# Optimization experiments

Hardware: AMD Instinct MI355X
Metric: run time of the kernel (lower is better)

## Reference

```python
import jax, jax.numpy as jnp
import numpy as np

HNUM = 64; WNUM = 64; TNUM = 2048; BIN_LEN = 0.01
B = 64; P = 512; VD = 128
VAP = 2.0; MINZ = 0.0; MAXZ = 2.0
LASER_ORIGIN = jnp.array([0.0, 0.0, -1.0], dtype=jnp.float32)
CAMERA_ORIGIN = jnp.array([0.05, 0.0, -1.0], dtype=jnp.float32)


def _wall_grid():
    ys = jnp.linspace(-1.0, 1.0, HNUM, dtype=jnp.float32)
    xs = jnp.linspace(-1.0, 1.0, WNUM, dtype=jnp.float32)
    gx, gy = jnp.meshgrid(xs, ys)  # [H, W]
    return jnp.stack([gx, gy, jnp.zeros_like(gx)], axis=-1)  # [H, W, 3] on wall z=0


def _normalize(v):
    n = jnp.linalg.norm(v, axis=-1, keepdims=True)
    return v / jnp.maximum(n, 1e-12)


def grid_sample_3d(vol, grid):
    # vol [D,H,W]; grid [N,3] (x,y,z) in [-1,1]; trilinear, zeros padding, align_corners=True
    D, H, W = vol.shape
    fx = (grid[:, 0] + 1.0) * 0.5 * (W - 1)
    fy = (grid[:, 1] + 1.0) * 0.5 * (H - 1)
    fz = (grid[:, 2] + 1.0) * 0.5 * (D - 1)
    x0 = jnp.floor(fx); y0 = jnp.floor(fy); z0 = jnp.floor(fz)
    wx = fx - x0; wy = fy - y0; wz = fz - z0
    x0 = x0.astype(jnp.int32); y0 = y0.astype(jnp.int32); z0 = z0.astype(jnp.int32)
    out = jnp.zeros(grid.shape[0], dtype=vol.dtype)
    for dz in (0, 1):
        for dy in (0, 1):
            for dx in (0, 1):
                ix = x0 + dx; iy = y0 + dy; iz = z0 + dz
                valid = (ix >= 0) & (ix < W) & (iy >= 0) & (iy < H) & (iz >= 0) & (iz < D)
                v = vol[jnp.clip(iz, 0, D - 1), jnp.clip(iy, 0, H - 1), jnp.clip(ix, 0, W - 1)]
                w = (wx if dx else 1.0 - wx) * (wy if dy else 1.0 - wy) * (wz if dz else 1.0 - wz)
                out = out + jnp.where(valid, v, 0.0) * w
    return out


def _forward(surf_pos, surf_normals, xys, phasor_volume, params_albedo,
             param_scale, param_sigma, param_lamda, param_dc):
    y_idx = xys[:, 0, 0]
    x_idx = xys[:, 0, 1]
    wall = _wall_grid()
    laser_pos = wall; camera_pos = wall
    d1 = jnp.linalg.norm(laser_pos - LASER_ORIGIN, axis=-1)  # [H,W]
    d4 = jnp.linalg.norm(camera_pos - CAMERA_ORIGIN, axis=-1)

    # --- albedo volume -> trilinear gather at surface points ---
    mask = (jax.lax.stop_gradient(phasor_volume) > 0.0).astype(jnp.float32)
    albedo_vol = jnp.clip(params_albedo * mask + phasor_volume * mask, 0.0, 1.0)
    z_scale = 2.0 / (MAXZ - MINZ)
    z_off = z_scale * (-MINZ) - 1.0
    g = jnp.stack([surf_pos[..., 0] * (2.0 / VAP),
                   -surf_pos[..., 1] * (2.0 / VAP),
                   surf_pos[..., 2] * z_scale + z_off], axis=-1).reshape(-1, 3)
    albedo_interp = grid_sample_3d(jnp.transpose(albedo_vol, (2, 0, 1)), g)
    albedo_interp = albedo_interp.reshape(surf_pos.shape[0], surf_pos.shape[1])  # [B,P]

    # --- per-point radiometry ---
    lp = laser_pos[y_idx, x_idx][:, None, :]   # [B,1,3]
    cp = camera_pos[y_idx, x_idx][:, None, :]
    lv = lp - surf_pos
    ld = jnp.linalg.norm(lv, axis=-1)          # [B,P]
    lvn = _normalize(lv)
    sv = cp - surf_pos
    sd = jnp.linalg.norm(sv, axis=-1)
    svn = _normalize(sv)
    # wall_normal = [0,0,1] => dot(v, n) = v_z
    value = (param_scale * albedo_interp / (ld ** 2 * sd ** 2)
             * (-lvn[..., 2]) * (-svn[..., 2])
             * jnp.sum(lvn * surf_normals, axis=-1)
             * jnp.sum(svn * surf_normals, axis=-1))  # [B,P]

    dist = d1[y_idx, x_idx][:, None] + ld + sd + d4[y_idx, x_idx][:, None]  # [B,P]
    axis_t = jnp.arange(TNUM, dtype=jnp.float32) * BIN_LEN
    sig2 = BIN_LEN ** 2 / (8.0 * np.log(2.0))
    # Gaussian splat of each point's time-of-flight into the transient histogram
    tdata = jnp.sum(value[..., None]
                    * jnp.exp(-(axis_t - dist[..., None]) ** 2 / (2.0 * sig2)), axis=1)  # [B,T]

    # --- impulse response: gaussian jitter (x) exponential SPAD response ---
    knum = TNUM // 4
    at = jnp.arange(knum, dtype=jnp.float32) - knum // 2
    sinv = 1.0 / param_sigma
    gauss = (sinv * (1.0 / jnp.sqrt(2.0 * jnp.pi))
             * jnp.exp(-at ** 2 * sinv ** 2 / 2.0))
    atc = jnp.maximum(at, 0.0)
    resp = param_lamda * jnp.exp(-param_lamda * atc)
    resp = jnp.where(jnp.arange(knum) < knum // 2, 0.0, resp)
    ir = jnp.convolve(gauss, resp, mode='same')
    tdata_out = jax.vmap(lambda r: jnp.convolve(r, ir, mode='same'))(tdata) + param_dc
    return tdata_out, tdata


def setup_inputs() -> dict:
    key = jax.random.key(0)
    k1, k2, k3, k4, k5 = jax.random.split(key, 5)
    sp = jax.random.uniform(k1, (B, P, 3), dtype=jnp.float32)
    surf_pos = sp * jnp.array([2.0, 2.0, 1.6]) + jnp.array([-1.0, -1.0, 0.2])
    surf_normals = jax.random.normal(k2, (B, P, 3), dtype=jnp.float32)
    surf_normals = surf_normals / jnp.maximum(
        jnp.linalg.norm(surf_normals, axis=-1, keepdims=True), 1e-12)
    xys = jax.random.randint(k3, (B, 1, 2), 0, HNUM).astype(jnp.int64)
    phasor_volume = jax.random.uniform(k4, (HNUM, WNUM, VD), dtype=jnp.float32)
    params_albedo = 0.1 * jax.random.uniform(k5, (HNUM, WNUM, VD), dtype=jnp.float32)
    return {
        'surf_pos': surf_pos,
        'surf_normals': surf_normals,
        'xys': xys,
        'phasor_volume': phasor_volume,
        'params_albedo': params_albedo,
        'param_scale': jnp.ones((1,), jnp.float32),
        'param_sigma': 0.8917 * jnp.ones((1,), jnp.float32),
        'param_lamda': 0.5 * jnp.ones((1,), jnp.float32),
        'param_dc': 1e-4 * jnp.ones((1,), jnp.float32),
    }


def reference(surf_pos, surf_normals, xys, phasor_volume, params_albedo,
              param_scale, param_sigma, param_lamda, param_dc):
    return _forward(surf_pos, surf_normals, xys, phasor_volume, params_albedo,
                    param_scale, param_sigma, param_lamda, param_dc)
```

## Files before the change

kernel.cpp:

```cpp
#include <hip/hip_runtime.h>
#include <math.h>

#define HNUM 64
#define WNUM 64
#define TNUM 2048
#define B_   64
#define P_   512
#define VD_  128
#define NSPLIT 4
#define NTAP 128
#define KOFF 240

#define LOG2E 1.44269504088896340736f

__global__ __launch_bounds__(128) void ptr_scatter_kernel(
    const float* __restrict__ surf_pos,
    const float* __restrict__ surf_norm,
    const int*   __restrict__ xys,
    const float* __restrict__ phasor,
    const float* __restrict__ albedo_p,
    const float* __restrict__ scale_p,
    const float* __restrict__ sigma_p,
    const float* __restrict__ lamda_p,
    float* __restrict__ ws)
{
    __shared__ float s_h[2048];
    const int tid = threadIdx.x;
    const int blk = blockIdx.x;

    if (blk == B_ * NSPLIT) {
        float* sA = s_h;
        float* sB = s_h + 128;
        const float sinv = 1.0f / sigma_p[0];
        const float lam  = lamda_p[0];
        const float eneg = __builtin_amdgcn_exp2f(-lam * LOG2E);
        const float at = (float)(tid - 17);
        const float g  = sinv * 0.3989422804014327f *
                         __builtin_amdgcn_exp2f(-0.5f * LOG2E * at * at * sinv * sinv);
        sA[tid] = (tid == 0) ? 0.0f : eneg;
        sB[tid] = lam * g;
        __syncthreads();
        #pragma unroll
        for (int d = 1; d < NTAP; d <<= 1) {
            float a = sA[tid], b = sB[tid], al = 1.0f, bl = 0.0f;
            if (tid >= d) { al = sA[tid - d]; bl = sB[tid - d]; }
            __syncthreads();
            if (tid >= d) { sA[tid] = a * al; sB[tid] = fmaf(a, bl, b); }
            __syncthreads();
        }
        ws[tid] = sB[tid];
        return;
    }

    const int b = blk >> 2, q = blk & 3;
    #pragma unroll
    for (int s = 0; s < 4; ++s)
        *reinterpret_cast<float4*>(&s_h[(tid + s * 128) * 4]) =
            make_float4(0.0f, 0.0f, 0.0f, 0.0f);
    __syncthreads();

    {
        const int p = q * 128 + tid;
        const int base = (b * P_ + p) * 3;
        const float px = surf_pos[base + 0];
        const float py = surf_pos[base + 1];
        const float pz = surf_pos[base + 2];
        const float nx = surf_norm[base + 0];
        const float ny = surf_norm[base + 1];
        const float nz = surf_norm[base + 2];

        const int y = xys[b * 2 + 0];
        const int x = xys[b * 2 + 1];
        const float wxp = -1.0f + 2.0f * (float)x / 63.0f;
        const float wyp = -1.0f + 2.0f * (float)y / 63.0f;
        const float d1  = sqrtf(wxp * wxp + wyp * wyp + 1.0f);
        const float dxc = wxp - 0.05f;
        const float d4  = sqrtf(dxc * dxc + wyp * wyp + 1.0f);
        const float scale = scale_p[0];

        const float fx = (px + 1.0f) * 31.5f;
        const float fy = (1.0f - py) * 31.5f;
        const float fz = pz * 63.5f;
        const float x0f = floorf(fx), y0f = floorf(fy), z0f = floorf(fz);
        const float wwx = fx - x0f, wwy = fy - y0f, wwz = fz - z0f;
        const int ix0 = (int)x0f, iy0 = (int)y0f, iz0 = (int)z0f;
        const int ix1 = min(ix0 + 1, WNUM - 1);
        const int iy1 = min(iy0 + 1, HNUM - 1);
        const int iz1 = iz0 + 1;

        float interp = 0.0f;
        #pragma unroll
        for (int c = 0; c < 8; ++c) {
            const int dx = c & 1, dy = (c >> 1) & 1, dz = c >> 2;
            const int ix = dx ? ix1 : ix0;
            const int iy = dy ? iy1 : iy0;
            const int iz = dz ? iz1 : iz0;
            const int idx = (iy * WNUM + ix) * VD_ + iz;
            const float ph = phasor[idx];
            const float al = albedo_p[idx];
            const float v  = (ph > 0.0f) ? fminf(fmaxf(al + ph, 0.0f), 1.0f) : 0.0f;
            const float w3 = (dx ? wwx : 1.0f - wwx) *
                             (dy ? wwy : 1.0f - wwy) *
                             (dz ? wwz : 1.0f - wwz);
            interp = fmaf(v, w3, interp);
        }

        const float lvx = wxp - px, lvy = wyp - py, lvz = -pz;
        const float ld2 = lvx * lvx + lvy * lvy + lvz * lvz;
        const float ld  = sqrtf(ld2);
        const float ild = 1.0f / fmaxf(ld, 1e-12f);
        const float lnz = lvz * ild;
        const float dotn = (lvx * nx + lvy * ny + lvz * nz) * ild;
        const float value = scale * interp / (ld2 * ld2) * (lnz * lnz) * (dotn * dotn);
        const float dist  = d1 + 2.0f * ld + d4;

        const float tc = dist * 100.0f;
        const int it0 = (int)floorf(tc) - 3;
        #pragma unroll
        for (int k = 0; k < 8; ++k) {
            const int t = it0 + k;
            if (t >= 0 && t < TNUM) {
                const float db = (float)t - tc;
                const float w = __builtin_amdgcn_exp2f(-4.0f * db * db);
                atomicAdd(&s_h[t], value * w);
            }
        }
    }
    __syncthreads();

    float* dst = ws + NTAP + blk * 2048;
    #pragma unroll
    for (int s = 0; s < 4; ++s) {
        const int i4 = (tid + s * 128) * 4;
        *reinterpret_cast<float4*>(&dst[i4]) =
            *reinterpret_cast<const float4*>(&s_h[i4]);
    }
}

__global__ __launch_bounds__(128) void ptr_conv_kernel(
    const float* __restrict__ ws,
    const float* __restrict__ dc_p,
    float* __restrict__ out,
    float* __restrict__ tdata)
{
    __shared__ float s_w[640];
    const int tid = threadIdx.x;
    const int b  = blockIdx.x >> 2;
    const int T0 = (blockIdx.x & 3) << 9;

    const float* part = ws + NTAP + (b * NSPLIT) * 2048;
    for (int idx = tid; idx < 160; idx += 128) {
        const int i = idx * 4;
        const int g = T0 - 112 + i;
        float4 v = make_float4(0.0f, 0.0f, 0.0f, 0.0f);
        if (g >= 0 && g < TNUM) {
            const float4 v0 = *reinterpret_cast<const float4*>(&part[g]);
            const float4 v1 = *reinterpret_cast<const float4*>(&part[2048 + g]);
            const float4 v2 = *reinterpret_cast<const float4*>(&part[4096 + g]);
            const float4 v3 = *reinterpret_cast<const float4*>(&part[6144 + g]);
            v.x = (v0.x + v1.x) + (v2.x + v3.x);
            v.y = (v0.y + v1.y) + (v2.y + v3.y);
            v.z = (v0.z + v1.z) + (v2.z + v3.z);
            v.w = (v0.w + v1.w) + (v2.w + v3.w);
        }
        *reinterpret_cast<float4*>(&s_w[i]) = v;
    }
    __syncthreads();

    const int l0 = tid * 4;
    *reinterpret_cast<float4*>(&tdata[b * TNUM + T0 + l0]) =
        *reinterpret_cast<const float4*>(&s_w[112 + l0]);

    const float4* irt4 = reinterpret_cast<const float4*>(ws);
    float acc0 = 0.0f, acc1 = 0.0f, acc2 = 0.0f, acc3 = 0.0f;
    float4 hi = *reinterpret_cast<const float4*>(&s_w[l0 + 128]);
    #pragma unroll
    for (int c = 0; c < 32; ++c) {
        const float4 lo  = *reinterpret_cast<const float4*>(&s_w[l0 + 124 - 4 * c]);
        const float4 irv = irt4[c];
        acc0 = fmaf(irv.x, lo.w, acc0); acc1 = fmaf(irv.x, hi.x, acc1);
        acc2 = fmaf(irv.x, hi.y, acc2); acc3 = fmaf(irv.x, hi.z, acc3);
        acc0 = fmaf(irv.y, lo.z, acc0); acc1 = fmaf(irv.y, lo.w, acc1);
        acc2 = fmaf(irv.y, hi.x, acc2); acc3 = fmaf(irv.y, hi.y, acc3);
        acc0 = fmaf(irv.z, lo.y, acc0); acc1 = fmaf(irv.z, lo.z, acc1);
        acc2 = fmaf(irv.z, lo.w, acc2); acc3 = fmaf(irv.z, hi.x, acc3);
        acc0 = fmaf(irv.w, lo.x, acc0); acc1 = fmaf(irv.w, lo.y, acc1);
        acc2 = fmaf(irv.w, lo.z, acc2); acc3 = fmaf(irv.w, lo.w, acc3);
        hi = lo;
    }

    const float dc = dc_p[0];
    float4 o;
    o.x = acc0 + dc; o.y = acc1 + dc; o.z = acc2 + dc; o.w = acc3 + dc;
    *reinterpret_cast<float4*>(&out[b * TNUM + T0 + l0]) = o;
}

extern "C" void kernel_launch(void* const* d_in, const int* in_sizes, int n_in,
                              void* d_out, int out_size, void* d_ws, size_t ws_size,
                              hipStream_t stream) {
    const float* surf_pos  = (const float*)d_in[0];
    const float* surf_norm = (const float*)d_in[1];
    const int*   xys       = (const int*)  d_in[2];
    const float* phasor    = (const float*)d_in[3];
    const float* albedo    = (const float*)d_in[4];
    const float* scale_p   = (const float*)d_in[5];
    const float* sigma_p   = (const float*)d_in[6];
    const float* lamda_p   = (const float*)d_in[7];
    const float* dc_p      = (const float*)d_in[8];

    float* out   = (float*)d_out;
    float* tdata = out + B_ * TNUM;
    float* ws    = (float*)d_ws;

    ptr_scatter_kernel<<<B_ * NSPLIT + 1, 128, 0, stream>>>(
        surf_pos, surf_norm, xys, phasor, albedo, scale_p, sigma_p, lamda_p, ws);
    ptr_conv_kernel<<<B_ * NSPLIT, 128, 0, stream>>>(ws, dc_p, out, tdata);
}
```

Before: 16.98 us.

## Fuse scatter and convolution into one kernel with per-block time windows

Merges the scatter and convolution kernels into a single launch. Each block of 512 threads handles one batch item and one 512-bin time slice. Every block recomputes the impulse-response prefix scan locally and tests all surface points of that item, doing the trilinear gather and the scatter only for points whose pulse lands in the slice window plus halo. This removes the second launch and the global workspace round-trip of partial histograms. In exchange the scan and the distance test are repeated in each of the four slice blocks.

Measured after the change: 23.98 us. +41.3%, slower.

```diff
diff --git a/kernel.cpp b/kernel.cpp
--- a/kernel.cpp
+++ b/kernel.cpp
@@ -7,13 +7,12 @@
 #define B_   64
 #define P_   512
 #define VD_  128
-#define NSPLIT 4
 #define NTAP 128
-#define KOFF 240
+#define WIN  640
 
 #define LOG2E 1.44269504088896340736f
 
-__global__ __launch_bounds__(128) void ptr_scatter_kernel(
+__global__ __launch_bounds__(512) void ptr_fused_kernel(
     const float* __restrict__ surf_pos,
     const float* __restrict__ surf_norm,
     const int*   __restrict__ xys,
@@ -22,53 +21,52 @@
     const float* __restrict__ scale_p,
     const float* __restrict__ sigma_p,
     const float* __restrict__ lamda_p,
-    float* __restrict__ ws)
+    const float* __restrict__ dc_p,
+    float* __restrict__ out,
+    float* __restrict__ tdata)
 {
-    __shared__ float s_h[2048];
+    __shared__ float s_w[WIN];
+    __shared__ float s_ir[NTAP];
+    __shared__ float sA[NTAP];
+    __shared__ float sB[NTAP];
+
     const int tid = threadIdx.x;
     const int blk = blockIdx.x;
+    const int b   = blk >> 2;
+    const int T0  = (blk & 3) << 9;
 
-    if (blk == B_ * NSPLIT) {
-        float* sA = s_h;
-        float* sB = s_h + 128;
-        const float sinv = 1.0f / sigma_p[0];
-        const float lam  = lamda_p[0];
-        const float eneg = __builtin_amdgcn_exp2f(-lam * LOG2E);
+    const int base = (b * P_ + tid) * 3;
+    const float px = surf_pos[base + 0];
+    const float py = surf_pos[base + 1];
+    const float pz = surf_pos[base + 2];
+
+    if (tid < WIN) s_w[tid] = 0.0f;
+    if (tid + 512 < WIN) s_w[tid + 512] = 0.0f;
+    const float sinv = 1.0f / sigma_p[0];
+    const float lam  = lamda_p[0];
+    const float eneg = __builtin_amdgcn_exp2f(-lam * LOG2E);
+    if (tid < NTAP) {
         const float at = (float)(tid - 17);
         const float g  = sinv * 0.3989422804014327f *
                          __builtin_amdgcn_exp2f(-0.5f * LOG2E * at * at * sinv * sinv);
         sA[tid] = (tid == 0) ? 0.0f : eneg;
         sB[tid] = lam * g;
+    }
+    __syncthreads();
+    #pragma unroll
+    for (int d = 1; d < NTAP; d <<= 1) {
+        float a = 0.0f, bv = 0.0f, al = 1.0f, bl = 0.0f;
+        if (tid < NTAP) {
+            a = sA[tid]; bv = sB[tid];
+            if (tid >= d) { al = sA[tid - d]; bl = sB[tid - d]; }
+        }
         __syncthreads();
-        #pragma unroll
-        for (int d = 1; d < NTAP; d <<= 1) {
-            float a = sA[tid], b = sB[tid], al = 1.0f, bl = 0.0f;
-            if (tid >= d) { al = sA[tid - d]; bl = sB[tid - d]; }
-            __syncthreads();
-            if (tid >= d) { sA[tid] = a * al; sB[tid] = fmaf(a, bl, b); }
-            __syncthreads();
-        }
-        ws[tid] = sB[tid];
-        return;
+        if (tid < NTAP && tid >= d) { sA[tid] = a * al; sB[tid] = fmaf(a, bl, bv); }
+        __syncthreads();
     }
-
-    const int b = blk >> 2, q = blk & 3;
-    #pragma unroll
-    for (int s = 0; s < 4; ++s)
-        *reinterpret_cast<float4*>(&s_h[(tid + s * 128) * 4]) =
-            make_float4(0.0f, 0.0f, 0.0f, 0.0f);
-    __syncthreads();
+    if (tid < NTAP) s_ir[tid] = sB[tid];
 
     {
-        const int p = q * 128 + tid;
-        const int base = (b * P_ + p) * 3;
-        const float px = surf_pos[base + 0];
-        const float py = surf_pos[base + 1];
-        const float pz = surf_pos[base + 2];
-        const float nx = surf_norm[base + 0];
-        const float ny = surf_norm[base + 1];
-        const float nz = surf_norm[base + 2];
-
         const int y = xys[b * 2 + 0];
         const int x = xys[b * 2 + 1];
         const float wxp = -1.0f + 2.0f * (float)x / 63.0f;
@@ -76,123 +74,93 @@
         const float d1  = sqrtf(wxp * wxp + wyp * wyp + 1.0f);
         const float dxc = wxp - 0.05f;
         const float d4  = sqrtf(dxc * dxc + wyp * wyp + 1.0f);
-        const float scale = scale_p[0];
-
-        const float fx = (px + 1.0f) * 31.5f;
-        const float fy = (1.0f - py) * 31.5f;
-        const float fz = pz * 63.5f;
-        const float x0f = floorf(fx), y0f = floorf(fy), z0f = floorf(fz);
-        const float wwx = fx - x0f, wwy = fy - y0f, wwz = fz - z0f;
-        const int ix0 = (int)x0f, iy0 = (int)y0f, iz0 = (int)z0f;
-        const int ix1 = min(ix0 + 1, WNUM - 1);
-        const int iy1 = min(iy0 + 1, HNUM - 1);
-        const int iz1 = iz0 + 1;
-
-        float interp = 0.0f;
-        #pragma unroll
-        for (int c = 0; c < 8; ++c) {
-            const int dx = c & 1, dy = (c >> 1) & 1, dz = c >> 2;
-            const int ix = dx ? ix1 : ix0;
-            const int iy = dy ? iy1 : iy0;
-            const int iz = dz ? iz1 : iz0;
-            const int idx = (iy * WNUM + ix) * VD_ + iz;
-            const float ph = phasor[idx];
-            const float al = albedo_p[idx];
-            const float v  = (ph > 0.0f) ? fminf(fmaxf(al + ph, 0.0f), 1.0f) : 0.0f;
-            const float w3 = (dx ? wwx : 1.0f - wwx) *
-                             (dy ? wwy : 1.0f - wwy) *
-                             (dz ? wwz : 1.0f - wwz);
-            interp = fmaf(v, w3, interp);
-        }
 
         const float lvx = wxp - px, lvy = wyp - py, lvz = -pz;
         const float ld2 = lvx * lvx + lvy * lvy + lvz * lvz;
         const float ld  = sqrtf(ld2);
-        const float ild = 1.0f / fmaxf(ld, 1e-12f);
-        const float lnz = lvz * ild;
-        const float dotn = (lvx * nx + lvy * ny + lvz * nz) * ild;
-        const float value = scale * interp / (ld2 * ld2) * (lnz * lnz) * (dotn * dotn);
-        const float dist  = d1 + 2.0f * ld + d4;
+        const float dist = d1 + 2.0f * ld + d4;
+        const float tc   = dist * 100.0f;
+        const int it0    = (int)floorf(tc) - 3;
 
-        const float tc = dist * 100.0f;
-        const int it0 = (int)floorf(tc) - 3;
-        #pragma unroll
-        for (int k = 0; k < 8; ++k) {
-            const int t = it0 + k;
-            if (t >= 0 && t < TNUM) {
-                const float db = (float)t - tc;
-                const float w = __builtin_amdgcn_exp2f(-4.0f * db * db);
-                atomicAdd(&s_h[t], value * w);
+        const int lo = max(0, T0 - 112);
+        const int hi = min(TNUM, T0 + 528);
+
+        if (it0 + 7 >= lo && it0 < hi) {
+            const float nx = surf_norm[base + 0];
+            const float ny = surf_norm[base + 1];
+            const float nz = surf_norm[base + 2];
+
+            const float fx = (px + 1.0f) * 31.5f;
+            const float fy = (1.0f - py) * 31.5f;
+            const float fz = pz * 63.5f;
+            const float x0f = floorf(fx), y0f = floorf(fy), z0f = floorf(fz);
+            const float wwx = fx - x0f, wwy = fy - y0f, wwz = fz - z0f;
+            const int ix0 = (int)x0f, iy0 = (int)y0f, iz0 = (int)z0f;
+            const int ix1 = min(ix0 + 1, WNUM - 1);
+            const int iy1 = min(iy0 + 1, HNUM - 1);
+            const int iz1 = iz0 + 1;
+
+            float interp = 0.0f;
+            #pragma unroll
+            for (int c = 0; c < 8; ++c) {
+                const int dx = c & 1, dy = (c >> 1) & 1, dz = c >> 2;
+                const int ix = dx ? ix1 : ix0;
+                const int iy = dy ? iy1 : iy0;
+                const int iz = dz ? iz1 : iz0;
+                const int idx = (iy * WNUM + ix) * VD_ + iz;
+                const float ph = phasor[idx];
+                const float al = albedo_p[idx];
+                const float v  = (ph > 0.0f) ? fminf(fmaxf(al + ph, 0.0f), 1.0f) : 0.0f;
+                const float w3 = (dx ? wwx : 1.0f - wwx) *
+                                 (dy ? wwy : 1.0f - wwy) *
+                                 (dz ? wwz : 1.0f - wwz);
+                interp = fmaf(v, w3, interp);
+            }
+
+            const float ild = 1.0f / fmaxf(ld, 1e-12f);
+            const float lnz = lvz * ild;
+            const float dotn = (lvx * nx + lvy * ny + lvz * nz) * ild;
+            const float value = scale_p[0] * interp / (ld2 * ld2) *
+                                (lnz * lnz) * (dotn * dotn);
+
+            #pragma unroll
+            for (int k = 0; k < 8; ++k) {
+                const int t = it0 + k;
+                if (t >= lo && t < hi) {
+                    const float db = (float)t - tc;
+                    const float w = __builtin_amdgcn_exp2f(-4.0f * db * db);
+                    atomicAdd(&s_w[t - (T0 - 112)], value * w);
+                }
             }
         }
     }
     __syncthreads();
 
-    float* dst = ws + NTAP + blk * 2048;
-    #pragma unroll
-    for (int s = 0; s < 4; ++s) {
-        const int i4 = (tid + s * 128) * 4;
-        *reinterpret_cast<float4*>(&dst[i4]) =
-            *reinterpret_cast<const float4*>(&s_h[i4]);
+    tdata[b * TNUM + T0 + tid] = s_w[112 + tid];
+
+    if (tid < 128) {
+        const int l0 = tid * 4;
+        float acc0 = 0.0f, acc1 = 0.0f, acc2 = 0.0f, acc3 = 0.0f;
+        float4 hi4 = *reinterpret_cast<const float4*>(&s_w[l0 + 128]);
+        #pragma unroll
+        for (int c = 0; c < 32; ++c) {
+            const float4 lo4 = *reinterpret_cast<const float4*>(&s_w[l0 + 124 - 4 * c]);
+            const float4 irv = *reinterpret_cast<const float4*>(&s_ir[4 * c]);
+            acc0 = fmaf(irv.x, lo4.w, acc0); acc1 = fmaf(irv.x, hi4.x, acc1);
+            acc2 = fmaf(irv.x, hi4.y, acc2); acc3 = fmaf(irv.x, hi4.z, acc3);
+            acc0 = fmaf(irv.y, lo4.z, acc0); acc1 = fmaf(irv.y, lo4.w, acc1);
+            acc2 = fmaf(irv.y, hi4.x, acc2); acc3 = fmaf(irv.y, hi4.y, acc3);
+            acc0 = fmaf(irv.z, lo4.y, acc0); acc1 = fmaf(irv.z, lo4.z, acc1);
+            acc2 = fmaf(irv.z, lo4.w, acc2); acc3 = fmaf(irv.z, hi4.x, acc3);
+            acc0 = fmaf(irv.w, lo4.x, acc0); acc1 = fmaf(irv.w, lo4.y, acc1);
+            acc2 = fmaf(irv.w, lo4.z, acc2); acc3 = fmaf(irv.w, lo4.w, acc3);
+            hi4 = lo4;
+        }
+        const float dc = dc_p[0];
+        float4 o;
+        o.x = acc0 + dc; o.y = acc1 + dc; o.z = acc2 + dc; o.w = acc3 + dc;
+        *reinterpret_cast<float4*>(&out[b * TNUM + T0 + l0]) = o;
     }
-}
-
-__global__ __launch_bounds__(128) void ptr_conv_kernel(
-    const float* __restrict__ ws,
-    const float* __restrict__ dc_p,
-    float* __restrict__ out,
-    float* __restrict__ tdata)
-{
-    __shared__ float s_w[640];
-    const int tid = threadIdx.x;
-    const int b  = blockIdx.x >> 2;
-    const int T0 = (blockIdx.x & 3) << 9;
-
-    const float* part = ws + NTAP + (b * NSPLIT) * 2048;
-    for (int idx = tid; idx < 160; idx += 128) {
-        const int i = idx * 4;
-        const int g = T0 - 112 + i;
-        float4 v = make_float4(0.0f, 0.0f, 0.0f, 0.0f);
-        if (g >= 0 && g < TNUM) {
-            const float4 v0 = *reinterpret_cast<const float4*>(&part[g]);
-            const float4 v1 = *reinterpret_cast<const float4*>(&part[2048 + g]);
-            const float4 v2 = *reinterpret_cast<const float4*>(&part[4096 + g]);
-            const float4 v3 = *reinterpret_cast<const float4*>(&part[6144 + g]);
-            v.x = (v0.x + v1.x) + (v2.x + v3.x);
-            v.y = (v0.y + v1.y) + (v2.y + v3.y);
-            v.z = (v0.z + v1.z) + (v2.z + v3.z);
-            v.w = (v0.w + v1.w) + (v2.w + v3.w);
-        }
-        *reinterpret_cast<float4*>(&s_w[i]) = v;
-    }
-    __syncthreads();
-
-    const int l0 = tid * 4;
-    *reinterpret_cast<float4*>(&tdata[b * TNUM + T0 + l0]) =
-        *reinterpret_cast<const float4*>(&s_w[112 + l0]);
-
-    const float4* irt4 = reinterpret_cast<const float4*>(ws);
-    float acc0 = 0.0f, acc1 = 0.0f, acc2 = 0.0f, acc3 = 0.0f;
-    float4 hi = *reinterpret_cast<const float4*>(&s_w[l0 + 128]);
-    #pragma unroll
-    for (int c = 0; c < 32; ++c) {
-        const float4 lo  = *reinterpret_cast<const float4*>(&s_w[l0 + 124 - 4 * c]);
-        const float4 irv = irt4[c];
-        acc0 = fmaf(irv.x, lo.w, acc0); acc1 = fmaf(irv.x, hi.x, acc1);
-        acc2 = fmaf(irv.x, hi.y, acc2); acc3 = fmaf(irv.x, hi.z, acc3);
-        acc0 = fmaf(irv.y, lo.z, acc0); acc1 = fmaf(irv.y, lo.w, acc1);
-        acc2 = fmaf(irv.y, hi.x, acc2); acc3 = fmaf(irv.y, hi.y, acc3);
-        acc0 = fmaf(irv.z, lo.y, acc0); acc1 = fmaf(irv.z, lo.z, acc1);
-        acc2 = fmaf(irv.z, lo.w, acc2); acc3 = fmaf(irv.z, hi.x, acc3);
-        acc0 = fmaf(irv.w, lo.x, acc0); acc1 = fmaf(irv.w, lo.y, acc1);
-        acc2 = fmaf(irv.w, lo.z, acc2); acc3 = fmaf(irv.w, lo.w, acc3);
-        hi = lo;
-    }
-
-    const float dc = dc_p[0];
-    float4 o;
-    o.x = acc0 + dc; o.y = acc1 + dc; o.z = acc2 + dc; o.w = acc3 + dc;
-    *reinterpret_cast<float4*>(&out[b * TNUM + T0 + l0]) = o;
 }
 
 extern "C" void kernel_launch(void* const* d_in, const int* in_sizes, int n_in,
@@ -210,9 +178,8 @@
 
     float* out   = (float*)d_out;
     float* tdata = out + B_ * TNUM;
-    float* ws    = (float*)d_ws;
 
-    ptr_scatter_kernel<<<B_ * NSPLIT + 1, 128, 0, stream>>>(
-        surf_pos, surf_norm, xys, phasor, albedo, scale_p, sigma_p, lamda_p, ws);
-    ptr_conv_kernel<<<B_ * NSPLIT, 128, 0, stream>>>(ws, dc_p, out, tdata);
+    ptr_fused_kernel<<<B_ * 4, 512, 0, stream>>>(
+        surf_pos, surf_norm, xys, phasor, albedo, scale_p, sigma_p, lamda_p,
+        dc_p, out, tdata);
 }
```
